# Optimization experiments

Hardware: AMD Instinct MI355X
Metric: run time of the kernel (lower is better)

Reference implementation:

```python
import jax, jax.numpy as jnp
import numpy as np

N = 100000      # nodes
E = 1600000     # edges
F_IN = 512      # num_features
H = 128         # hidden
C = 40          # num_classes
K = 10          # Chebyshev order


def setup_inputs() -> dict:
    key = jax.random.key(0)
    ks = jax.random.split(key, 6)
    x = jax.random.normal(ks[0], (N, F_IN), dtype=jnp.float32)
    edge_index = jax.random.randint(ks[1], (2, E), 0, N, dtype=jnp.int32)
    W1 = jax.random.normal(ks[2], (F_IN, H), dtype=jnp.float32) / np.sqrt(F_IN).astype(np.float32)
    b1 = jnp.zeros((H,), dtype=jnp.float32)
    W2 = jax.random.normal(ks[3], (H, C), dtype=jnp.float32) / np.sqrt(H).astype(np.float32)
    b2 = jnp.zeros((C,), dtype=jnp.float32)
    # Chebyshev coefficients temp[K+1]
    temp = 1.0 + 0.1 * jax.random.normal(ks[4], (K + 1,), dtype=jnp.float32)
    return {"x": x, "edge_index": edge_index, "W1": W1, "b1": b1, "W2": W2, "b2": b2, "temp": temp}


def reference(x, edge_index, W1, b1, W2, b2, temp):
    # MLP encoder (eval mode: dropout is identity)
    h = jax.nn.relu(x @ W1 + b1)          # [N, H]
    h = h @ W2 + b2                        # [N, C]

    # gcn_norm: add self-loops, symmetric normalization
    self_loop = jnp.arange(N, dtype=edge_index.dtype)
    row = jnp.concatenate([edge_index[0], self_loop])   # [E+N]
    col = jnp.concatenate([edge_index[1], self_loop])
    deg = jax.ops.segment_sum(jnp.ones_like(row, dtype=jnp.float32), row, num_segments=N)
    dis = jnp.where(deg > 0, jax.lax.rsqrt(jnp.maximum(deg, 1.0)), 0.0)
    norm = dis[row] * dis[col]             # [E+N]

    def prop(v):  # A_hat @ v : gather-scale-scatter over edges
        return jax.ops.segment_sum(norm[:, None] * v[col], row, num_segments=N)

    # Chebyshev recurrence: Tx_k = 2*A_hat*Tx_{k-1} - Tx_{k-2}
    Tx0 = h
    Tx1 = prop(h)
    out0 = temp[0] * Tx0 + temp[1] * Tx1

    def body(carry, coe):
        t0, t1, acc = carry
        t2 = 2.0 * prop(t1) - t0
        return (t1, t2, acc + coe * t2), None

    (_, _, out), _ = jax.lax.scan(body, (Tx0, Tx1, out0), temp[2:])
    return jax.nn.log_softmax(out, axis=1)
```

## Files before the change

### kernel.cpp

```cpp
#include <hip/hip_runtime.h>
#include <hip/hip_bf16.h>
#include <cstdint>
#include <cstddef>

#define NN   100000
#define EE   1600000
#define FIN  512
#define HID  128
#define CC   40
#define KORD 10
#define SHB  80

typedef __attribute__((ext_vector_type(4))) float f4;
typedef __attribute__((ext_vector_type(2))) float f2;
typedef __attribute__((ext_vector_type(8))) short short8_t;
typedef __attribute__((ext_vector_type(4))) unsigned int u4;

__device__ __forceinline__ unsigned short cvt_bf16(float f) {
  union { float f; unsigned u; } a; a.f = f;
  unsigned r = a.u + 0x7fffu + ((a.u >> 16) & 1u);
  return (unsigned short)(r >> 16);
}
__device__ __forceinline__ unsigned pk_bf(float a, float b) {
  union { float f; unsigned u; } x, y; x.f = a; y.f = b;
  unsigned ra = x.u + 0x7fffu + ((x.u >> 16) & 1u);
  unsigned rb = y.u + 0x7fffu + ((y.u >> 16) & 1u);
  return (ra >> 16) | (rb & 0xffff0000u);
}
__device__ __forceinline__ f4 cvf2(unsigned lo, unsigned hi) {
  union { unsigned u; float f; } a, b, c, d;
  a.u = lo << 16; b.u = lo & 0xffff0000u;
  c.u = hi << 16; d.u = hi & 0xffff0000u;
  f4 r; r.x = a.f; r.y = b.f; r.z = c.f; r.w = d.f; return r;
}

__global__ __launch_bounds__(256) void k_dw(const int* __restrict__ rowI, int* __restrict__ deg,
                                            const float* __restrict__ W1, unsigned short* __restrict__ W1T,
                                            int ndeg) {
  int b = blockIdx.x;
  if (b < ndeg) {
    int i = b * 256 + threadIdx.x;
    if (i < EE) atomicAdd(&deg[rowI[i]], 1);
  } else {
    int idx = (b - ndeg) * 256 + threadIdx.x;
    int k = idx >> 7, n = idx & 127;
    W1T[(k >> 5) * 4096 + n * 32 + (k & 31)] = cvt_bf16(W1[idx]);
  }
}

__global__ __launch_bounds__(256) void k_finalize(int* __restrict__ deg, float* __restrict__ dis,
                                                  float* __restrict__ sqd, float* __restrict__ invd) {
  int i = blockIdx.x * 256 + threadIdx.x;
  if (i < NN) {
    int d = deg[i] + 1;
    deg[i] = d;
    float fd = (float)d;
    dis[i]  = rsqrtf(fd);
    sqd[i]  = sqrtf(fd);
    invd[i] = 1.0f / fd;
  }
}

__global__ __launch_bounds__(256) void k_scan1(const int* __restrict__ cnt, int* __restrict__ excl,
                                               int* __restrict__ bsums) {
  __shared__ int s[256];
  int tid = threadIdx.x;
  int base = blockIdx.x * 1024 + tid * 4;
  int v0 = (base + 0 < NN) ? cnt[base + 0] : 0;
  int v1 = (base + 1 < NN) ? cnt[base + 1] : 0;
  int v2 = (base + 2 < NN) ? cnt[base + 2] : 0;
  int v3 = (base + 3 < NN) ? cnt[base + 3] : 0;
  int tsum = v0 + v1 + v2 + v3;
  s[tid] = tsum;
  __syncthreads();
  for (int off = 1; off < 256; off <<= 1) {
    int t = (tid >= off) ? s[tid - off] : 0;
    __syncthreads();
    if (tid >= off) s[tid] += t;
    __syncthreads();
  }
  int run = s[tid] - tsum;
  if (tid == 255) bsums[blockIdx.x] = s[255];
  if (base + 0 < NN) excl[base + 0] = run; run += v0;
  if (base + 1 < NN) excl[base + 1] = run; run += v1;
  if (base + 2 < NN) excl[base + 2] = run; run += v2;
  if (base + 3 < NN) excl[base + 3] = run;
}

__global__ __launch_bounds__(128) void k_scan2(int* __restrict__ bsums, int nb) {
  __shared__ int s[128];
  int tid = threadIdx.x;
  int v = (tid < nb) ? bsums[tid] : 0;
  s[tid] = v;
  __syncthreads();
  for (int off = 1; off < 128; off <<= 1) {
    int t = (tid >= off) ? s[tid - off] : 0;
    __syncthreads();
    if (tid >= off) s[tid] += t;
    __syncthreads();
  }
  if (tid < nb) bsums[tid] = s[tid] - v;
}

__global__ __launch_bounds__(256) void k_scan3(const int* __restrict__ cnt, int* __restrict__ rs,
                                               int* __restrict__ cur, const int* __restrict__ bsums) {
  int i = blockIdx.x * 256 + threadIdx.x;
  if (i < NN) {
    int v = rs[i] + bsums[i >> 10];
    rs[i] = v;
    cur[i] = v;
    if (i == NN - 1) rs[NN] = v + cnt[i];
  }
}

#define SLICE_ROWS (NN / 8)
#define SC_CHUNK   2048
__global__ __launch_bounds__(256) void k_scatter(const int* __restrict__ rowI, const int* __restrict__ colI,
                                                 int* __restrict__ cur, int* __restrict__ colS) {
  int slice = blockIdx.x & 7;
  int chunk = blockIdx.x >> 3;
  int lo = slice * SLICE_ROWS, hi = lo + SLICE_ROWS;
#pragma unroll
  for (int t = 0; t < SC_CHUNK / 256; ++t) {
    int i = chunk * SC_CHUNK + t * 256 + threadIdx.x;
    if (i < EE + NN) {
      int r = (i < EE) ? rowI[i] : (i - EE);
      if (r >= lo && r < hi) {
        int c = (i < EE) ? colI[i] : r;
        int pos = atomicAdd(&cur[r], 1);
        colS[pos] = c * SHB;
      }
    }
  }
}

#define LDK 40
__global__ __launch_bounds__(256) void k_gemm1(const float* __restrict__ x, const unsigned short* __restrict__ W1T,
                                               const float* __restrict__ b1, float* __restrict__ h1) {
  __shared__ __align__(16) short As_s[128][LDK];
  __shared__ __align__(16) short Bs_s[128][LDK];
  int tid  = threadIdx.x;
  int wave = tid >> 6, lane = tid & 63;
  int blockRow = blockIdx.x * 128;
  int wr = (wave & 1) * 64, wc = (wave >> 1) * 64;
  int l15 = lane & 15, lk = (lane >> 4) * 8;
  int ar = tid >> 1, ak = (tid & 1) * 16;

  f4 acc[4][4] = {};

  for (int k0 = 0; k0 < FIN; k0 += 32) {
    int gr = blockRow + ar;
    f4 xv0 = {0.f,0.f,0.f,0.f}, xv1 = xv0, xv2 = xv0, xv3 = xv0;
    if (gr < NN) {
      const float* xr = x + (size_t)gr * FIN + k0 + ak;
      xv0 = *(const f4*)&xr[0];
      xv1 = *(const f4*)&xr[4];
      xv2 = *(const f4*)&xr[8];
      xv3 = *(const f4*)&xr[12];
    }
    short8_t p0, p1;
#pragma unroll
    for (int q = 0; q < 4; ++q) {
      p0[q]     = (short)cvt_bf16(xv0[q]);
      p0[q + 4] = (short)cvt_bf16(xv1[q]);
      p1[q]     = (short)cvt_bf16(xv2[q]);
      p1[q + 4] = (short)cvt_bf16(xv3[q]);
    }
    *(short8_t*)&As_s[ar][ak]     = p0;
    *(short8_t*)&As_s[ar][ak + 8] = p1;

    const unsigned short* Wt = W1T + (k0 >> 5) * 4096;
    short8_t q0 = *(const short8_t*)&Wt[tid * 16];
    short8_t q1 = *(const short8_t*)&Wt[tid * 16 + 8];
    int bn = tid >> 1, bkk = (tid & 1) * 16;
    *(short8_t*)&Bs_s[bn][bkk]     = q0;
    *(short8_t*)&Bs_s[bn][bkk + 8] = q1;

    __syncthreads();

    short8_t afr[4], bfr[4];
#pragma unroll
    for (int m = 0; m < 4; ++m) afr[m] = *(const short8_t*)&As_s[wr + m * 16 + l15][lk];
#pragma unroll
    for (int n = 0; n < 4; ++n) bfr[n] = *(const short8_t*)&Bs_s[wc + n * 16 + l15][lk];
#pragma unroll
    for (int m = 0; m < 4; ++m)
#pragma unroll
      for (int n = 0; n < 4; ++n)
        acc[m][n] = __builtin_amdgcn_mfma_f32_16x16x32_bf16(afr[m], bfr[n], acc[m][n], 0, 0, 0);

    __syncthreads();
  }

  float bias[4];
#pragma unroll
  for (int n = 0; n < 4; ++n) bias[n] = b1[wc + n * 16 + l15];
#pragma unroll
  for (int m = 0; m < 4; ++m) {
    int baseRow = blockRow + wr + m * 16 + (lane >> 4) * 4;
#pragma unroll
    for (int n = 0; n < 4; ++n) {
      int col = wc + n * 16 + l15;
#pragma unroll
      for (int r = 0; r < 4; ++r) {
        int grow = baseRow + r;
        if (grow < NN) h1[(size_t)grow * HID + col] = fmaxf(acc[m][n][r] + bias[n], 0.f);
      }
    }
  }
}

__global__ __launch_bounds__(256) void k_gemm2(const float* __restrict__ h1, const float* __restrict__ W2,
                                               const float* __restrict__ b2, const float* __restrict__ temp,
                                               const float* __restrict__ dis,
                                               unsigned short* __restrict__ sh0, float* __restrict__ outAcc) {
  __shared__ float sW[HID * CC];
  __shared__ float sb[CC];
  int tid = threadIdx.x;
  for (int i = tid; i < HID * CC; i += 256) sW[i] = W2[i];
  if (tid < CC) sb[tid] = b2[tid];
  __syncthreads();
  int gid = blockIdx.x * 256 + tid;
  if (gid >= NN * 20) return;
  int row = gid / 20;
  int c2  = (gid - row * 20) * 2;
  const float* hr = h1 + (size_t)row * HID;
  float a0 = sb[c2], a1 = sb[c2 + 1];
#pragma unroll 8
  for (int k = 0; k < HID; ++k) {
    float hv = hr[k];
    a0 = fmaf(hv, sW[k * CC + c2], a0);
    a1 = fmaf(hv, sW[k * CC + c2 + 1], a1);
  }
  float t0v = temp[0];
  f2 ov; ov.x = t0v * a0; ov.y = t0v * a1;
  *(f2*)&outAcc[(size_t)row * CC + c2] = ov;
  float dv = dis[row];
  *(unsigned*)((char*)sh0 + (size_t)row * SHB + c2 * 2) = pk_bf(a0 * dv, a1 * dv);
}

template <int MODE>
__global__ __launch_bounds__(256) void k_prop(const unsigned short* __restrict__ shIn,
                                              unsigned short* __restrict__ shOut,
                                              float* __restrict__ outAcc,
                                              const int* __restrict__ colS,
                                              const int* __restrict__ rs,
                                              const float* __restrict__ invd, const float* __restrict__ sqd,
                                              const float* __restrict__ temp, int kIdx) {
  int lane = threadIdx.x & 63;
  int wave = threadIdx.x >> 6;
  int grp  = lane / 5;
  int fi   = lane - grp * 5;
  int node = blockIdx.x * 48 + wave * 12 + grp;
  bool active = (grp < 12) && (node < NN);
  int s = 0, e = 0;
  if (active) { s = rs[node]; e = rs[node + 1]; }
  const char* base = (const char*)shIn + fi * 16;
  f4 lo0 = {0.f,0.f,0.f,0.f}, hi0 = lo0, lo1 = lo0, hi1 = lo0;
  f4 lo2 = lo0, hi2 = lo0, lo3 = lo0, hi3 = lo0;
  int j = s;
  for (; j + 4 <= e; j += 4) {
    int c0 = colS[j], c1 = colS[j + 1], c2 = colS[j + 2], c3 = colS[j + 3];
    u4 p0 = *(const u4*)(base + c0);
    u4 p1 = *(const u4*)(base + c1);
    u4 p2 = *(const u4*)(base + c2);
    u4 p3 = *(const u4*)(base + c3);
    lo0 += cvf2(p0.x, p0.y); hi0 += cvf2(p0.z, p0.w);
    lo1 += cvf2(p1.x, p1.y); hi1 += cvf2(p1.z, p1.w);
    lo2 += cvf2(p2.x, p2.y); hi2 += cvf2(p2.z, p2.w);
    lo3 += cvf2(p3.x, p3.y); hi3 += cvf2(p3.z, p3.w);
  }
  if (j + 2 <= e) {
    int c0 = colS[j], c1 = colS[j + 1];
    u4 p0 = *(const u4*)(base + c0);
    u4 p1 = *(const u4*)(base + c1);
    lo0 += cvf2(p0.x, p0.y); hi0 += cvf2(p0.z, p0.w);
    lo1 += cvf2(p1.x, p1.y); hi1 += cvf2(p1.z, p1.w);
    j += 2;
  }
  if (j < e) {
    u4 p0 = *(const u4*)(base + colS[j]);
    lo2 += cvf2(p0.x, p0.y); hi2 += cvf2(p0.z, p0.w);
  }

  if (active) {
    f4 slo = (lo0 + lo1) + (lo2 + lo3);
    f4 shi = (hi0 + hi1) + (hi2 + hi3);
    float iv = invd[node];
    float ts = temp[kIdx] * sqd[node];
    char* shp = (char*)shOut + (size_t)node * SHB + fi * 16;
    f4 wlo, whi;
    if (MODE == 0) {
      wlo = iv * slo; whi = iv * shi;
    } else {
      u4 pp = *(const u4*)shp;
      f4 plo = cvf2(pp.x, pp.y), phi = cvf2(pp.z, pp.w);
      wlo = (2.f * iv) * slo - plo;
      whi = (2.f * iv) * shi - phi;
    }
    u4 pk;
    pk.x = pk_bf(wlo.x, wlo.y); pk.y = pk_bf(wlo.z, wlo.w);
    pk.z = pk_bf(whi.x, whi.y); pk.w = pk_bf(whi.z, whi.w);
    *(u4*)shp = pk;
    size_t o = (size_t)node * CC + fi * 8;
    f4 olo = *(const f4*)&outAcc[o];
    f4 ohi = *(const f4*)&outAcc[o + 4];
    *(f4*)&outAcc[o]     = olo + ts * wlo;
    *(f4*)&outAcc[o + 4] = ohi + ts * whi;
  }
}

__global__ __launch_bounds__(256) void k_lsm(float* __restrict__ out) {
  int row = blockIdx.x * 256 + threadIdx.x;
  if (row >= NN) return;
  float* p = out + (size_t)row * CC;
  float v[CC];
#pragma unroll
  for (int i = 0; i < CC / 4; ++i) *(f4*)&v[i * 4] = *(const f4*)&p[i * 4];
  float m = v[0];
#pragma unroll
  for (int i = 1; i < CC; ++i) m = fmaxf(m, v[i]);
  float ssum = 0.f;
#pragma unroll
  for (int i = 0; i < CC; ++i) ssum += expf(v[i] - m);
  float lse = m + logf(ssum);
#pragma unroll
  for (int i = 0; i < CC; ++i) v[i] -= lse;
#pragma unroll
  for (int i = 0; i < CC / 4; ++i) *(f4*)&p[i * 4] = *(f4*)&v[i * 4];
}

extern "C" void kernel_launch(void* const* d_in, const int* in_sizes, int n_in,
                              void* d_out, int out_size, void* d_ws, size_t ws_size,
                              hipStream_t stream) {
  const float* x    = (const float*)d_in[0];
  const int*   ei   = (const int*)d_in[1];
  const float* W1   = (const float*)d_in[2];
  const float* b1   = (const float*)d_in[3];
  const float* W2   = (const float*)d_in[4];
  const float* b2   = (const float*)d_in[5];
  const float* temp = (const float*)d_in[6];
  const int* rowI = ei;
  const int* colI = ei + EE;
  float* out = (float*)d_out;

  char* w = (char*)d_ws;
  auto alloc = [&](size_t bytes) -> void* {
    void* p = (void*)w;
    w += (bytes + 255) & ~(size_t)255;
    return p;
  };
  int*   deg   = (int*)  alloc((size_t)NN * 4);
  float* dis   = (float*)alloc((size_t)NN * 4);
  float* sqd   = (float*)alloc((size_t)NN * 4);
  float* invd  = (float*)alloc((size_t)NN * 4);
  int*   rs    = (int*)  alloc((size_t)(NN + 1) * 4);
  int*   cur   = (int*)  alloc((size_t)NN * 4);
  int*   bsums = (int*)  alloc(512 * 4);
  unsigned short* W1T = (unsigned short*)alloc((size_t)FIN * HID * 2);
  unsigned short* sh0 = (unsigned short*)alloc((size_t)NN * SHB);
  unsigned short* sh1 = (unsigned short*)alloc((size_t)NN * SHB);
  int*   colS  = (int*)  alloc((size_t)(EE + NN) * 4);
  float* h1    = (float*)alloc((size_t)NN * HID * 4);

  hipMemsetAsync(deg, 0, (size_t)NN * 4, stream);

  const int NDEG = (EE + 255) / 256;
  const int NW1T = FIN * HID / 256;
  k_dw<<<NDEG + NW1T, 256, 0, stream>>>(rowI, deg, W1, W1T, NDEG);

  k_finalize<<<(NN + 255) / 256, 256, 0, stream>>>(deg, dis, sqd, invd);

  int nb = (NN + 1023) / 1024;
  k_scan1<<<nb, 256, 0, stream>>>(deg, rs, bsums);
  k_scan2<<<1, 128, 0, stream>>>(bsums, nb);
  k_scan3<<<(NN + 255) / 256, 256, 0, stream>>>(deg, rs, cur, bsums);

  const int NCH = (EE + NN + SC_CHUNK - 1) / SC_CHUNK;
  k_scatter<<<8 * NCH, 256, 0, stream>>>(rowI, colI, cur, colS);

  k_gemm1<<<(NN + 127) / 128, 256, 0, stream>>>(x, W1T, b1, h1);
  k_gemm2<<<(NN * 20 + 255) / 256, 256, 0, stream>>>(h1, W2, b2, temp, dis, sh0, out);

  int G = (NN + 47) / 48;
  unsigned short* sh[2] = {sh0, sh1};
  k_prop<0><<<G, 256, 0, stream>>>(sh[0], sh[1], out, colS, rs, invd, sqd, temp, 1);
  for (int k = 2; k <= KORD; ++k) {
    k_prop<1><<<G, 256, 0, stream>>>(sh[(k - 1) & 1], sh[k & 1], out, colS, rs, invd, sqd, temp, k);
  }

  k_lsm<<<(NN + 255) / 256, 256, 0, stream>>>(out);
}
```

Baseline: 666.7 us.

## Store all Chebyshev terms in bf16 and combine them with log-softmax in one final pass

Each propagation step no longer reads and writes the fp32 output accumulator. Instead every Chebyshev term T_k is kept in its own bf16 buffer, and a single final kernel forms the temp-weighted sum, scales it by sqrt(deg), and applies log-softmax using wave shuffles across the five-lane group. This cuts per-step fp32 read-modify-write traffic and merges the separate log-softmax kernel into the combine pass. In exchange it needs about 11x the workspace for the term buffers, and the final sum is built from bf16-rounded terms.

After: 633.9 us. 1.05x faster.

```diff
diff --git a/kernel.cpp b/kernel.cpp
--- a/kernel.cpp
+++ b/kernel.cpp
@@ -10,9 +10,9 @@
 #define CC   40
 #define KORD 10
 #define SHB  80
+#define SHSTRIDE ((size_t)NN * SHB)
 
 typedef __attribute__((ext_vector_type(4))) float f4;
-typedef __attribute__((ext_vector_type(2))) float f2;
 typedef __attribute__((ext_vector_type(8))) short short8_t;
 typedef __attribute__((ext_vector_type(4))) unsigned int u4;
 
@@ -213,7 +213,7 @@
 __global__ __launch_bounds__(256) void k_gemm2(const float* __restrict__ h1, const float* __restrict__ W2,
                                                const float* __restrict__ b2, const float* __restrict__ temp,
                                                const float* __restrict__ dis,
-                                               unsigned short* __restrict__ sh0, float* __restrict__ outAcc) {
+                                               unsigned short* __restrict__ sh0) {
   __shared__ float sW[HID * CC];
   __shared__ float sb[CC];
   int tid = threadIdx.x;
@@ -232,21 +232,17 @@
     a0 = fmaf(hv, sW[k * CC + c2], a0);
     a1 = fmaf(hv, sW[k * CC + c2 + 1], a1);
   }
-  float t0v = temp[0];
-  f2 ov; ov.x = t0v * a0; ov.y = t0v * a1;
-  *(f2*)&outAcc[(size_t)row * CC + c2] = ov;
   float dv = dis[row];
   *(unsigned*)((char*)sh0 + (size_t)row * SHB + c2 * 2) = pk_bf(a0 * dv, a1 * dv);
 }
 
 template <int MODE>
 __global__ __launch_bounds__(256) void k_prop(const unsigned short* __restrict__ shIn,
+                                              const unsigned short* __restrict__ shPrev,
                                               unsigned short* __restrict__ shOut,
-                                              float* __restrict__ outAcc,
                                               const int* __restrict__ colS,
                                               const int* __restrict__ rs,
-                                              const float* __restrict__ invd, const float* __restrict__ sqd,
-                                              const float* __restrict__ temp, int kIdx) {
+                                              const float* __restrict__ invd) {
   int lane = threadIdx.x & 63;
   int wave = threadIdx.x >> 6;
   int grp  = lane / 5;
@@ -287,13 +283,12 @@
     f4 slo = (lo0 + lo1) + (lo2 + lo3);
     f4 shi = (hi0 + hi1) + (hi2 + hi3);
     float iv = invd[node];
-    float ts = temp[kIdx] * sqd[node];
-    char* shp = (char*)shOut + (size_t)node * SHB + fi * 16;
+    size_t ro = (size_t)node * SHB + fi * 16;
     f4 wlo, whi;
     if (MODE == 0) {
       wlo = iv * slo; whi = iv * shi;
     } else {
-      u4 pp = *(const u4*)shp;
+      u4 pp = *(const u4*)((const char*)shPrev + ro);
       f4 plo = cvf2(pp.x, pp.y), phi = cvf2(pp.z, pp.w);
       wlo = (2.f * iv) * slo - plo;
       whi = (2.f * iv) * shi - phi;
@@ -301,33 +296,49 @@
     u4 pk;
     pk.x = pk_bf(wlo.x, wlo.y); pk.y = pk_bf(wlo.z, wlo.w);
     pk.z = pk_bf(whi.x, whi.y); pk.w = pk_bf(whi.z, whi.w);
-    *(u4*)shp = pk;
-    size_t o = (size_t)node * CC + fi * 8;
-    f4 olo = *(const f4*)&outAcc[o];
-    f4 ohi = *(const f4*)&outAcc[o + 4];
-    *(f4*)&outAcc[o]     = olo + ts * wlo;
-    *(f4*)&outAcc[o + 4] = ohi + ts * whi;
-  }
-}
-
-__global__ __launch_bounds__(256) void k_lsm(float* __restrict__ out) {
-  int row = blockIdx.x * 256 + threadIdx.x;
-  if (row >= NN) return;
-  float* p = out + (size_t)row * CC;
-  float v[CC];
-#pragma unroll
-  for (int i = 0; i < CC / 4; ++i) *(f4*)&v[i * 4] = *(const f4*)&p[i * 4];
-  float m = v[0];
-#pragma unroll
-  for (int i = 1; i < CC; ++i) m = fmaxf(m, v[i]);
-  float ssum = 0.f;
-#pragma unroll
-  for (int i = 0; i < CC; ++i) ssum += expf(v[i] - m);
-  float lse = m + logf(ssum);
-#pragma unroll
-  for (int i = 0; i < CC; ++i) v[i] -= lse;
-#pragma unroll
-  for (int i = 0; i < CC / 4; ++i) *(f4*)&p[i * 4] = *(f4*)&v[i * 4];
+    *(u4*)((char*)shOut + ro) = pk;
+  }
+}
+
+__global__ __launch_bounds__(256) void k_comb(const unsigned short* __restrict__ shBase,
+                                              float* __restrict__ outF,
+                                              const float* __restrict__ sqd,
+                                              const float* __restrict__ temp) {
+  int lane = threadIdx.x & 63;
+  int wave = threadIdx.x >> 6;
+  int grp  = lane / 5;
+  int fi   = lane - grp * 5;
+  int node = blockIdx.x * 48 + wave * 12 + grp;
+  if (grp >= 12 || node >= NN) return;
+
+  const char* p = (const char*)shBase + (size_t)node * SHB + fi * 16;
+  f4 alo = {0.f,0.f,0.f,0.f}, ahi = alo;
+#pragma unroll
+  for (int k = 0; k <= KORD; ++k) {
+    u4 pp = *(const u4*)(p + (size_t)k * SHSTRIDE);
+    float tk = temp[k];
+    alo += tk * cvf2(pp.x, pp.y);
+    ahi += tk * cvf2(pp.z, pp.w);
+  }
+  float sq = sqd[node];
+  alo *= sq; ahi *= sq;
+
+  int gb = grp * 5;
+  float m = fmaxf(fmaxf(fmaxf(alo.x, alo.y), fmaxf(alo.z, alo.w)),
+                  fmaxf(fmaxf(ahi.x, ahi.y), fmaxf(ahi.z, ahi.w)));
+  float mm = m;
+#pragma unroll
+  for (int j = 0; j < 5; ++j) mm = fmaxf(mm, __shfl(m, gb + j));
+  float ss = expf(alo.x - mm) + expf(alo.y - mm) + expf(alo.z - mm) + expf(alo.w - mm)
+           + expf(ahi.x - mm) + expf(ahi.y - mm) + expf(ahi.z - mm) + expf(ahi.w - mm);
+  float tot = 0.f;
+#pragma unroll
+  for (int j = 0; j < 5; ++j) tot += __shfl(ss, gb + j);
+  float lse = mm + logf(tot);
+  alo -= lse; ahi -= lse;
+  size_t o = (size_t)node * CC + fi * 8;
+  *(f4*)&outF[o]     = alo;
+  *(f4*)&outF[o + 4] = ahi;
 }
 
 extern "C" void kernel_launch(void* const* d_in, const int* in_sizes, int n_in,
@@ -358,10 +369,13 @@
   int*   cur   = (int*)  alloc((size_t)NN * 4);
   int*   bsums = (int*)  alloc(512 * 4);
   unsigned short* W1T = (unsigned short*)alloc((size_t)FIN * HID * 2);
-  unsigned short* sh0 = (unsigned short*)alloc((size_t)NN * SHB);
-  unsigned short* sh1 = (unsigned short*)alloc((size_t)NN * SHB);
+  unsigned short* shAll = (unsigned short*)alloc(SHSTRIDE * (KORD + 1));
   int*   colS  = (int*)  alloc((size_t)(EE + NN) * 4);
   float* h1    = (float*)alloc((size_t)NN * HID * 4);
+
+  auto sh = [&](int k) -> unsigned short* {
+    return (unsigned short*)((char*)shAll + (size_t)k * SHSTRIDE);
+  };
 
   hipMemsetAsync(deg, 0, (size_t)NN * 4, stream);
 
@@ -380,14 +394,13 @@
   k_scatter<<<8 * NCH, 256, 0, stream>>>(rowI, colI, cur, colS);
 
   k_gemm1<<<(NN + 127) / 128, 256, 0, stream>>>(x, W1T, b1, h1);
-  k_gemm2<<<(NN * 20 + 255) / 256, 256, 0, stream>>>(h1, W2, b2, temp, dis, sh0, out);
+  k_gemm2<<<(NN * 20 + 255) / 256, 256, 0, stream>>>(h1, W2, b2, temp, dis, sh(0));
 
   int G = (NN + 47) / 48;
-  unsigned short* sh[2] = {sh0, sh1};
-  k_prop<0><<<G, 256, 0, stream>>>(sh[0], sh[1], out, colS, rs, invd, sqd, temp, 1);
+  k_prop<0><<<G, 256, 0, stream>>>(sh(0), sh(0), sh(1), colS, rs, invd);
   for (int k = 2; k <= KORD; ++k) {
-    k_prop<1><<<G, 256, 0, stream>>>(sh[(k - 1) & 1], sh[k & 1], out, colS, rs, invd, sqd, temp, k);
-  }
-
-  k_lsm<<<(NN + 255) / 256, 256, 0, stream>>>(out);
-}
+    k_prop<1><<<G, 256, 0, stream>>>(sh(k - 1), sh(k - 2), sh(k), colS, rs, invd);
+  }
+
+  k_comb<<<G, 256, 0, stream>>>(shAll, out, sqd, temp);
+}
```
